# Kernel tuning notes

Measured on AMD Instinct MI355X. Metric: run time of the kernel, lower is better.

Reference implementation:

```python
import jax, jax.numpy as jnp
import numpy as np

V, B, T, D, H, HS, L, F = 50257, 16, 256, 64, 4, 16, 4, 256
EPS = 1e-5


def layernorm(x, g, b):
    mu = jnp.mean(x, axis=-1, keepdims=True)
    var = jnp.var(x, axis=-1, keepdims=True)
    return (x - mu) * jax.lax.rsqrt(var + EPS) * g + b


def setup_inputs() -> dict:
    key = jax.random.key(0)
    ks = jax.random.split(key, 20)
    s = 0.02
    inp = {
        "idx": jax.random.randint(ks[0], (B, T), 0, V),
        "targets": jax.random.randint(ks[1], (B, T), 0, V),
        "tok_emb": jax.random.normal(ks[2], (V, D), jnp.float32) * s,
        "pos_emb": jax.random.normal(ks[3], (T, D), jnp.float32) * s,
        "Wq": jax.random.normal(ks[4], (L, H, D, HS), jnp.float32) * s,
        "Wk": jax.random.normal(ks[5], (L, H, D, HS), jnp.float32) * s,
        "Wv": jax.random.normal(ks[6], (L, H, D, HS), jnp.float32) * s,
        "Wo": jax.random.normal(ks[7], (L, D, D), jnp.float32) * s,
        "bo": jnp.zeros((L, D), jnp.float32),
        "ln1_g": jnp.ones((L, D), jnp.float32),
        "ln1_b": jnp.zeros((L, D), jnp.float32),
        "ln2_g": jnp.ones((L, D), jnp.float32),
        "ln2_b": jnp.zeros((L, D), jnp.float32),
        "W1": jax.random.normal(ks[8], (L, D, F), jnp.float32) * s,
        "b1": jnp.zeros((L, F), jnp.float32),
        "W2": jax.random.normal(ks[9], (L, F, D), jnp.float32) * s,
        "b2": jnp.zeros((L, D), jnp.float32),
        "lnf_g": jnp.ones((D,), jnp.float32),
        "lnf_b": jnp.zeros((D,), jnp.float32),
        "Whead": jax.random.normal(ks[10], (D, V), jnp.float32) * s,
        "bhead": jnp.zeros((V,), jnp.float32),
    }
    return inp


def reference(idx, targets, tok_emb, pos_emb, Wq, Wk, Wv, Wo, bo,
              ln1_g, ln1_b, ln2_g, ln2_b, W1, b1, W2, b2,
              lnf_g, lnf_b, Whead, bhead):
    Tt = idx.shape[1]
    x = tok_emb[idx] + pos_emb[:Tt]  # [B,T,D]
    causal = jnp.tril(jnp.ones((Tt, Tt), bool))
    for l in range(L):
        h = layernorm(x, ln1_g[l], ln1_b[l])
        q = jnp.einsum('btd,hds->bhts', h, Wq[l])
        k = jnp.einsum('btd,hds->bhts', h, Wk[l])
        v = jnp.einsum('btd,hds->bhts', h, Wv[l])
        # NOTE: original applies NO 1/sqrt(head_size) scaling
        scores = jnp.einsum('bhts,bhus->bhtu', q, k)  # [B,H,T,T]
        scores = jnp.where(causal, scores, -jnp.inf)
        attn = jax.nn.softmax(scores, axis=-1)
        o = jnp.einsum('bhtu,bhus->bths', attn, v)  # [B,T,H,HS]
        o = o.reshape(o.shape[0], Tt, D)
        x = x + o @ Wo[l] + bo[l]
        h2 = layernorm(x, ln2_g[l], ln2_b[l])
        x = x + jax.nn.relu(h2 @ W1[l] + b1[l]) @ W2[l] + b2[l]
    x = layernorm(x, lnf_g, lnf_b)
    logits = x @ Whead + bhead  # [B,T,V]
    logp = jax.nn.log_softmax(logits, axis=-1)
    loss = -jnp.mean(jnp.take_along_axis(logp, targets[..., None], axis=-1))
    return (logits, loss)
```

## Files before the change

### kernel.cpp

```cpp
#include <hip/hip_runtime.h>
#include <hip/hip_bf16.h>
#include <math.h>

constexpr int NV  = 50257;
constexpr int NB  = 16;
constexpr int NT  = 256;
constexpr int ND  = 64;
constexpr int NH  = 4;
constexpr int NHS = 16;
constexpr int NL  = 4;
constexpr int NF  = 256;
constexpr int NN  = NB * NT;
constexpr float EPS = 1e-5f;

constexpr int NCB2 = 200;
constexpr int NVP  = NCB2 * 256;
constexpr int LOGITS = NN * NV;
constexpr int RB_N  = NN / 64;
constexpr int CB_PER_XCD = NCB2 / 8;

constexpr int X_OFF   = 0;
constexpr int Q_OFF   = X_OFF  + NN * ND;
constexpr int K_OFF   = Q_OFF  + NN * ND;
constexpr int V_OFF   = K_OFF  + NN * ND;
constexpr int O_OFF   = V_OFF  + NN * ND;
constexpr int A_OFF   = O_OFF  + NN * ND;
constexpr int XFB_OFF = A_OFF  + NN * NF;
constexpr int WM_OFF  = XFB_OFF + NN * ND / 2;
constexpr int WS2_OFF = WM_OFF + 200 * NN;
constexpr int WHB_OFF = WS2_OFF + 200 * NN;
constexpr int LP_OFF  = WHB_OFF + NVP * 32;

typedef __bf16 bf16x8 __attribute__((ext_vector_type(8)));
typedef float  f32x4  __attribute__((ext_vector_type(4)));

__global__ __launch_bounds__(256) void k_ln_qkv(
        float* __restrict__ x, const float* __restrict__ g, const float* __restrict__ bb,
        const float* __restrict__ Wq, const float* __restrict__ Wk, const float* __restrict__ Wv,
        __hip_bfloat16* __restrict__ q, __hip_bfloat16* __restrict__ k,
        __hip_bfloat16* __restrict__ v,
        const int* __restrict__ idx, const float* __restrict__ tok,
        const float* __restrict__ pos) {
    __shared__ float hs[16][65];
    int t = threadIdx.x;
    int r0 = blockIdx.x * 16;
    for (int i = t; i < 16 * 64; i += 256) {
        int n = r0 + (i >> 6);
        int tt = n & (NT - 1), d = i & 63;
        float e = tok[idx[n] * ND + d] + pos[tt * ND + d];
        hs[i >> 6][i & 63] = e;
        x[(size_t)r0 * 64 + i] = e;
    }
    __syncthreads();
    {
        int row = t >> 4, sub = t & 15;
        float s = 0.f, s2 = 0.f;
        #pragma unroll
        for (int j = 0; j < 4; j++) { float vv = hs[row][sub * 4 + j]; s += vv; s2 += vv * vv; }
        #pragma unroll
        for (int off = 1; off < 16; off <<= 1) { s += __shfl_xor(s, off); s2 += __shfl_xor(s2, off); }
        float mu = s * (1.f / 64.f);
        float var = s2 * (1.f / 64.f) - mu * mu;
        float rs = rsqrtf(var + EPS);
        #pragma unroll
        for (int j = 0; j < 4; j++) {
            int d = sub * 4 + j;
            hs[row][d] = (hs[row][d] - mu) * rs * g[d] + bb[d];
        }
    }
    __syncthreads();
    int c = t & 63, rg = t >> 6;
    int head = c >> 4, sidx = c & 15;
    float aq[4], ak[4], av[4];
    #pragma unroll
    for (int i = 0; i < 4; i++) { aq[i] = 0.f; ak[i] = 0.f; av[i] = 0.f; }
    for (int kk = 0; kk < 64; kk++) {
        float wq = Wq[(head * 64 + kk) * 16 + sidx];
        float wk = Wk[(head * 64 + kk) * 16 + sidx];
        float wv = Wv[(head * 64 + kk) * 16 + sidx];
        #pragma unroll
        for (int i = 0; i < 4; i++) {
            float h = hs[rg * 4 + i][kk];
            aq[i] += h * wq; ak[i] += h * wk; av[i] += h * wv;
        }
    }
    #pragma unroll
    for (int i = 0; i < 4; i++) {
        int n = r0 + rg * 4 + i;
        int b = n >> 8, tt = n & 255;
        int oidx = ((b * NH + head) * NT + tt) * NHS + sidx;
        q[oidx] = __float2bfloat16(aq[i]);
        k[oidx] = __float2bfloat16(ak[i]);
        v[oidx] = __float2bfloat16(av[i]);
    }
}

__global__ __launch_bounds__(256) void k_attn(
        const __hip_bfloat16* __restrict__ q, const __hip_bfloat16* __restrict__ k,
        const __hip_bfloat16* __restrict__ v, float* __restrict__ o) {
    __shared__ __bf16 ks[256][24];
    __shared__ __bf16 vt[16][264];
    __shared__ __bf16 ps[4][16][40];

    int blk = blockIdx.x;
    int bh = blk >> 2, tq = blk & 3;
    int t = threadIdx.x;
    int w = t >> 6, l = t & 63;
    int lr = l & 15, lg = l >> 4;
    int nrows = tq * 64 + 64;

    const __hip_bfloat16* kbp = k + (size_t)bh * NT * NHS;
    const __hip_bfloat16* vbp = v + (size_t)bh * NT * NHS;
    for (int r = t; r < nrows; r += 256) {
        const uint4* src = (const uint4*)(kbp + r * 16);
        uint4 k0 = src[0], k1 = src[1];
        *(uint4*)&ks[r][0] = k0;
        *(uint4*)&ks[r][8] = k1;
        const uint4* vsrc = (const uint4*)(vbp + r * 16);
        union { uint4 u[2]; __bf16 h[16]; } vu;
        vu.u[0] = vsrc[0]; vu.u[1] = vsrc[1];
        #pragma unroll
        for (int hh = 0; hh < 16; hh++)
            vt[hh][r] = vu.h[hh];
    }
    __syncthreads();

    bf16x8 zero8;
    #pragma unroll
    for (int e = 0; e < 8; e++) zero8[e] = (__bf16)0.0f;

    int qb = tq * 64 + w * 16;
    bf16x8 qf = zero8;
    if (lg < 2)
        qf = *reinterpret_cast<const bf16x8*>(q + ((size_t)bh * NT + qb + lr) * 16 + lg * 8);

    int ntiles = tq * 4 + w + 1;
    f32x4 oacc = {0.f, 0.f, 0.f, 0.f};
    float lsum[4] = {0.f, 0.f, 0.f, 0.f};

    for (int kt = 0; kt < ntiles; kt++) {
        int kb2 = kt * 16;
        bool diag = (kt == ntiles - 1);

        bf16x8 kf = zero8;
        if (lg < 2)
            kf = *reinterpret_cast<const bf16x8*>(&ks[kb2 + lr][lg * 8]);

        f32x4 s4 = {0.f, 0.f, 0.f, 0.f};
        s4 = __builtin_amdgcn_mfma_f32_16x16x32_bf16(qf, kf, s4, 0, 0, 0);

        #pragma unroll
        for (int reg = 0; reg < 4; reg++) {
            float pv = __expf(s4[reg]);
            if (diag && lr > lg * 4 + reg) pv = 0.f;
            lsum[reg] += pv;
            ps[w][lg * 4 + reg][lr] = (__bf16)pv;
        }

        bf16x8 pf = zero8, vf = zero8;
        if (lg < 2) {
            pf = *reinterpret_cast<const bf16x8*>(&ps[w][lr][lg * 8]);
            vf = *reinterpret_cast<const bf16x8*>(&vt[lr][kb2 + lg * 8]);
        }
        oacc = __builtin_amdgcn_mfma_f32_16x16x32_bf16(pf, vf, oacc, 0, 0, 0);
    }

    #pragma unroll
    for (int reg = 0; reg < 4; reg++) {
        float e = lsum[reg];
        #pragma unroll
        for (int off = 1; off < 16; off <<= 1) e += __shfl_xor(e, off);
        lsum[reg] = e;
    }

    int b = bh >> 2, h = bh & 3;
    #pragma unroll
    for (int reg = 0; reg < 4; reg++) {
        int qrow = qb + lg * 4 + reg;
        o[((size_t)b * NT + qrow) * ND + h * NHS + lr] = oacc[reg] / lsum[reg];
    }
}

__global__ __launch_bounds__(256) void k_post(
        const float* __restrict__ o, const float* __restrict__ Wo, const float* __restrict__ bo,
        const float* __restrict__ g2, const float* __restrict__ bg2,
        const float* __restrict__ W1, const float* __restrict__ b1,
        const float* __restrict__ W2, const float* __restrict__ b2m,
        float* __restrict__ x,
        const float* __restrict__ g1n, const float* __restrict__ b1n,
        const float* __restrict__ Wqn, const float* __restrict__ Wkn,
        const float* __restrict__ Wvn,
        __hip_bfloat16* __restrict__ q, __hip_bfloat16* __restrict__ k,
        __hip_bfloat16* __restrict__ v,
        const float* __restrict__ lg, const float* __restrict__ lb,
        __hip_bfloat16* __restrict__ xfb, int last) {
    __shared__ float os[16][65];
    __shared__ float xs[16][65];
    __shared__ float as[16][257];
    int t = threadIdx.x;
    int r0 = blockIdx.x * 16;
    for (int i = t; i < 16 * 64; i += 256)
        os[i >> 6][i & 63] = o[r0 * 64 + i];
    __syncthreads();
    int c = t & 63, rg = t >> 6;
    {
        float pr[4] = {0.f, 0.f, 0.f, 0.f};
        for (int kk = 0; kk < 64; kk++) {
            float w = Wo[kk * 64 + c];
            #pragma unroll
            for (int i = 0; i < 4; i++) pr[i] += os[rg * 4 + i][kk] * w;
        }
        float bias = bo[c];
        #pragma unroll
        for (int i = 0; i < 4; i++) {
            int row = rg * 4 + i;
            xs[row][c] = x[(r0 + row) * 64 + c] + pr[i] + bias;
        }
    }
    __syncthreads();
    {
        int row = t >> 4, sub = t & 15;
        float s = 0.f, s2 = 0.f;
        #pragma unroll
        for (int j = 0; j < 4; j++) { float vv = xs[row][sub * 4 + j]; s += vv; s2 += vv * vv; }
        #pragma unroll
        for (int off = 1; off < 16; off <<= 1) { s += __shfl_xor(s, off); s2 += __shfl_xor(s2, off); }
        float mu = s * (1.f / 64.f);
        float var = s2 * (1.f / 64.f) - mu * mu;
        float rs = rsqrtf(var + EPS);
        #pragma unroll
        for (int j = 0; j < 4; j++) {
            int d = sub * 4 + j;
            os[row][d] = (xs[row][d] - mu) * rs * g2[d] + bg2[d];
        }
    }
    __syncthreads();
    {
        float m1[16];
        #pragma unroll
        for (int i = 0; i < 16; i++) m1[i] = 0.f;
        for (int kk = 0; kk < 64; kk++) {
            float w = W1[kk * NF + t];
            #pragma unroll
            for (int i = 0; i < 16; i++) m1[i] += os[i][kk] * w;
        }
        float bb1 = b1[t];
        #pragma unroll
        for (int i = 0; i < 16; i++) as[i][t] = fmaxf(m1[i] + bb1, 0.f);
    }
    __syncthreads();
    {
        float m2[4] = {0.f, 0.f, 0.f, 0.f};
        for (int kk = 0; kk < 256; kk++) {
            float w = W2[kk * 64 + c];
            #pragma unroll
            for (int i = 0; i < 4; i++) m2[i] += as[rg * 4 + i][kk] * w;
        }
        float bias = b2m[c];
        #pragma unroll
        for (int i = 0; i < 4; i++) {
            int row = rg * 4 + i;
            xs[row][c] += m2[i] + bias;
        }
    }
    __syncthreads();

    if (last) {
        int row = t >> 4, sub = t & 15;
        float s = 0.f, s2 = 0.f;
        #pragma unroll
        for (int j = 0; j < 4; j++) { float vv = xs[row][sub * 4 + j]; s += vv; s2 += vv * vv; }
        #pragma unroll
        for (int off = 1; off < 16; off <<= 1) { s += __shfl_xor(s, off); s2 += __shfl_xor(s2, off); }
        float mu = s * (1.f / 64.f);
        float var = s2 * (1.f / 64.f) - mu * mu;
        float rs = rsqrtf(var + EPS);
        #pragma unroll
        for (int j = 0; j < 4; j++) {
            int d = sub * 4 + j;
            float val = (xs[row][d] - mu) * rs * lg[d] + lb[d];
            xfb[(r0 + row) * 64 + d] = __float2bfloat16(val);
        }
        return;
    }

    {
        #pragma unroll
        for (int i = 0; i < 4; i++) {
            int row = rg * 4 + i;
            x[(r0 + row) * 64 + c] = xs[row][c];
        }
    }
    {
        int row = t >> 4, sub = t & 15;
        float s = 0.f, s2 = 0.f;
        #pragma unroll
        for (int j = 0; j < 4; j++) { float vv = xs[row][sub * 4 + j]; s += vv; s2 += vv * vv; }
        #pragma unroll
        for (int off = 1; off < 16; off <<= 1) { s += __shfl_xor(s, off); s2 += __shfl_xor(s2, off); }
        float mu = s * (1.f / 64.f);
        float var = s2 * (1.f / 64.f) - mu * mu;
        float rs = rsqrtf(var + EPS);
        #pragma unroll
        for (int j = 0; j < 4; j++) {
            int d = sub * 4 + j;
            os[row][d] = (xs[row][d] - mu) * rs * g1n[d] + b1n[d];
        }
    }
    __syncthreads();
    {
        int head = c >> 4, sidx = c & 15;
        float aq[4], ak[4], av[4];
        #pragma unroll
        for (int i = 0; i < 4; i++) { aq[i] = 0.f; ak[i] = 0.f; av[i] = 0.f; }
        for (int kk = 0; kk < 64; kk++) {
            float wq = Wqn[(head * 64 + kk) * 16 + sidx];
            float wk = Wkn[(head * 64 + kk) * 16 + sidx];
            float wv = Wvn[(head * 64 + kk) * 16 + sidx];
            #pragma unroll
            for (int i = 0; i < 4; i++) {
                float h = os[rg * 4 + i][kk];
                aq[i] += h * wq; ak[i] += h * wk; av[i] += h * wv;
            }
        }
        #pragma unroll
        for (int i = 0; i < 4; i++) {
            int n = r0 + rg * 4 + i;
            int b = n >> 8, tt = n & 255;
            int oidx = ((b * NH + head) * NT + tt) * NHS + sidx;
            q[oidx] = __float2bfloat16(aq[i]);
            k[oidx] = __float2bfloat16(ak[i]);
            v[oidx] = __float2bfloat16(av[i]);
        }
    }
}

__global__ __launch_bounds__(256) void k_convW(
        const float* __restrict__ Wh, __hip_bfloat16* __restrict__ whb) {
    __shared__ float w[64][65];
    int t = threadIdx.x;
    int n0 = blockIdx.x * 64;
    for (int i = t; i < 64 * 64; i += 256) {
        int k = i >> 6, c = i & 63;
        int n = n0 + c;
        w[k][c] = (n < NV) ? Wh[k * NV + n] : 0.f;
    }
    __syncthreads();
    int c = t >> 2, kq = t & 3;
    int n = n0 + c;
    union { __hip_bfloat16 h[16]; uint4 u[2]; } pk;
    #pragma unroll
    for (int j = 0; j < 16; j++)
        pk.h[j] = __float2bfloat16(w[kq * 16 + j][c]);
    uint4* dst = (uint4*)(whb + (size_t)n * 64 + kq * 16);
    dst[0] = pk.u[0];
    dst[1] = pk.u[1];
}

__global__ __launch_bounds__(256) void k_head(
        const __hip_bfloat16* __restrict__ xfb, const __hip_bfloat16* __restrict__ whb,
        const float* __restrict__ bhead, float* __restrict__ out,
        float* __restrict__ wsum) {
    __shared__ float ssm[4][64];

    int i0 = blockIdx.x;
    int xcd = i0 & 7;
    int j  = i0 >> 3;
    int rb = j / CB_PER_XCD;
    int cb = xcd * CB_PER_XCD + (j - rb * CB_PER_XCD);

    int t = threadIdx.x;
    int w = t >> 6, l = t & 63;
    int lr = l & 15, lg = l >> 4;
    int r0 = rb * 64;
    int cw = cb * 256 + w * 64;
    int c4 = cw + lr * 4;

    bf16x8 a[4][2], b[4][2];
    {
        const __hip_bfloat16* ap = xfb + (size_t)(r0 + lr) * 64 + lg * 8;
        #pragma unroll
        for (int m = 0; m < 4; m++)
            #pragma unroll
            for (int ks = 0; ks < 2; ks++)
                a[m][ks] = *reinterpret_cast<const bf16x8*>(ap + m * 16 * 64 + ks * 32);
        const __hip_bfloat16* bp = whb + (size_t)c4 * 64 + lg * 8;
        #pragma unroll
        for (int n = 0; n < 4; n++)
            #pragma unroll
            for (int ks = 0; ks < 2; ks++)
                b[n][ks] = *reinterpret_cast<const bf16x8*>(bp + n * 64 + ks * 32);
    }

    f32x4 acc[4][4];
    #pragma unroll
    for (int m = 0; m < 4; m++)
        #pragma unroll
        for (int n = 0; n < 4; n++)
            #pragma unroll
            for (int j2 = 0; j2 < 4; j2++) acc[m][n][j2] = 0.f;

    #pragma unroll
    for (int ks = 0; ks < 2; ks++)
        #pragma unroll
        for (int m = 0; m < 4; m++)
            #pragma unroll
            for (int n = 0; n < 4; n++)
                acc[m][n] = __builtin_amdgcn_mfma_f32_16x16x32_bf16(a[m][ks], b[n][ks], acc[m][n], 0, 0, 0);

    bool all4 = (c4 + 3 < NV);
    float bias[4];
    bool  cok[4];
    if (all4) {
        float4 bv = *(const float4*)(bhead + c4);
        bias[0] = bv.x; bias[1] = bv.y; bias[2] = bv.z; bias[3] = bv.w;
        cok[0] = cok[1] = cok[2] = cok[3] = true;
    } else {
        #pragma unroll
        for (int n = 0; n < 4; n++) {
            int gc = c4 + n;
            cok[n] = (gc < NV);
            bias[n] = cok[n] ? bhead[gc] : 0.f;
        }
    }

    float es[16];
    #pragma unroll
    for (int m = 0; m < 4; m++) {
        #pragma unroll
        for (int i = 0; i < 4; i++) {
            int rl = 4 * lg + i;
            int grow = r0 + m * 16 + rl;
            float vals[4];
            float e = 0.f;
            #pragma unroll
            for (int n = 0; n < 4; n++) {
                float v = acc[m][n][i] + bias[n];
                vals[n] = v;
                if (cok[n]) e += __expf(v);
            }
            es[m * 4 + i] = e;
            float* dst = out + (size_t)grow * NV + c4;
            if (all4) {
                f32x4 vv = {vals[0], vals[1], vals[2], vals[3]};
                __builtin_nontemporal_store(vv, (f32x4*)dst);
            } else {
                #pragma unroll
                for (int n = 0; n < 4; n++)
                    if (cok[n]) __builtin_nontemporal_store(vals[n], dst + n);
            }
        }
    }

    #pragma unroll
    for (int m = 0; m < 4; m++) {
        #pragma unroll
        for (int i = 0; i < 4; i++) {
            float e = es[m * 4 + i];
            #pragma unroll
            for (int off = 1; off < 16; off <<= 1) e += __shfl_xor(e, off);
            if (lr == 0) ssm[w][m * 16 + 4 * lg + i] = e;
        }
    }

    __syncthreads();
    if (t < 64)
        wsum[cb * NN + r0 + t] = ssm[0][t] + ssm[1][t] + ssm[2][t] + ssm[3][t];
}

__global__ void k_loss1(const float* __restrict__ wsum,
                        const float* __restrict__ out, const int* __restrict__ targets,
                        float* __restrict__ lp) {
    int row = blockIdx.x * blockDim.x + threadIdx.x;
    if (row >= NN) return;
    float S = 0.f;
    for (int cb = 0; cb < NCB2; cb++)
        S += wsum[cb * NN + row];
    float lse = logf(S);
    int tg = targets[row];
    float lt = out[(size_t)row * NV + tg];
    lp[row] = lt - lse;
}

__global__ void k_loss2(const float* __restrict__ lp, float* __restrict__ out) {
    __shared__ float red[4];
    int t = threadIdx.x;
    float s = 0.f;
    for (int i = t; i < NN; i += 256) s += lp[i];
    for (int off = 1; off < 64; off <<= 1) s += __shfl_xor(s, off);
    if ((t & 63) == 0) red[t >> 6] = s;
    __syncthreads();
    if (t == 0) {
        float tot = red[0] + red[1] + red[2] + red[3];
        out[LOGITS] = -tot / (float)NN;
    }
}

extern "C" void kernel_launch(void* const* d_in, const int* in_sizes, int n_in,
                              void* d_out, int out_size, void* d_ws, size_t ws_size,
                              hipStream_t stream) {
    const int*   idx     = (const int*)d_in[0];
    const int*   targets = (const int*)d_in[1];
    const float* tok     = (const float*)d_in[2];
    const float* pos     = (const float*)d_in[3];
    const float* Wq      = (const float*)d_in[4];
    const float* Wk      = (const float*)d_in[5];
    const float* Wv      = (const float*)d_in[6];
    const float* Wo      = (const float*)d_in[7];
    const float* bo      = (const float*)d_in[8];
    const float* ln1g    = (const float*)d_in[9];
    const float* ln1b    = (const float*)d_in[10];
    const float* ln2g    = (const float*)d_in[11];
    const float* ln2b    = (const float*)d_in[12];
    const float* W1      = (const float*)d_in[13];
    const float* b1      = (const float*)d_in[14];
    const float* W2      = (const float*)d_in[15];
    const float* b2      = (const float*)d_in[16];
    const float* lnfg    = (const float*)d_in[17];
    const float* lnfb    = (const float*)d_in[18];
    const float* Wh      = (const float*)d_in[19];
    const float* bhead   = (const float*)d_in[20];

    float* ws = (float*)d_ws;
    float* x  = ws + X_OFF;
    __hip_bfloat16* q = (__hip_bfloat16*)(ws + Q_OFF);
    __hip_bfloat16* k = (__hip_bfloat16*)(ws + K_OFF);
    __hip_bfloat16* v = (__hip_bfloat16*)(ws + V_OFF);
    float* o  = ws + O_OFF;
    __hip_bfloat16* xfb = (__hip_bfloat16*)(ws + XFB_OFF);
    float* wsm = ws + WS2_OFF;
    __hip_bfloat16* whb = (__hip_bfloat16*)(ws + WHB_OFF);
    float* lp  = ws + LP_OFF;
    float* out = (float*)d_out;

    k_convW<<<NVP / 64, 256, 0, stream>>>(Wh, whb);

    k_ln_qkv<<<NN / 16, 256, 0, stream>>>(x, ln1g, ln1b, Wq, Wk, Wv, q, k, v,
                                          idx, tok, pos);

    for (int l = 0; l < NL; l++) {
        int last = (l == NL - 1) ? 1 : 0;
        int ln = last ? l : l + 1;
        k_attn<<<NB * NH * 4, 256, 0, stream>>>(q, k, v, o);
        k_post<<<NN / 16, 256, 0, stream>>>(o, Wo + l * ND * ND, bo + l * ND,
                                            ln2g + l * ND, ln2b + l * ND,
                                            W1 + l * ND * NF, b1 + l * NF,
                                            W2 + l * NF * ND, b2 + l * ND, x,
                                            ln1g + ln * ND, ln1b + ln * ND,
                                            Wq + ln * NH * ND * NHS,
                                            Wk + ln * NH * ND * NHS,
                                            Wv + ln * NH * ND * NHS,
                                            q, k, v,
                                            lnfg, lnfb, xfb, last);
    }

    k_head<<<NCB2 * RB_N, 256, 0, stream>>>(xfb, whb, bhead, out, wsm);

    k_loss1<<<NN / 256, 256, 0, stream>>>(wsm, out, targets, lp);
    k_loss2<<<1, 256, 0, stream>>>(lp, out);
}
```

Baseline: 495.5 us.

## Fuse attention into per-layer kernel with ping-pong QKV buffers and transposed V

Merges the separate attention kernel into the post-attention MLP kernel, so each 16-row block computes its own causal attention straight from global K/V. Q/K/V are double-buffered across layers to avoid races, and V is stored transposed so the PV MFMA operand loads are contiguous. This removes one launch per layer and the fp32 attention-output round trip through global memory. The cost is redundant K/V reads, since there is no LDS staging and each block rereads the K/V prefix. The head kernel also swaps nontemporal stores for plain stores and replaces the shuffle reduction with an LDS reduction.

After: 504.9 us. About the same (+1.9%).

```diff
diff --git a/kernel.cpp b/kernel.cpp
--- a/kernel.cpp
+++ b/kernel.cpp
@@ -25,6 +25,9 @@
 constexpr int V_OFF   = K_OFF  + NN * ND;
 constexpr int O_OFF   = V_OFF  + NN * ND;
 constexpr int A_OFF   = O_OFF  + NN * ND;
+constexpr int Q2_OFF  = O_OFF;
+constexpr int K2_OFF  = O_OFF + NN * ND / 2;
+constexpr int V2_OFF  = A_OFF;
 constexpr int XFB_OFF = A_OFF  + NN * NF;
 constexpr int WM_OFF  = XFB_OFF + NN * ND / 2;
 constexpr int WS2_OFF = WM_OFF + 200 * NN;
@@ -71,6 +74,7 @@
     __syncthreads();
     int c = t & 63, rg = t >> 6;
     int head = c >> 4, sidx = c & 15;
+    int b = r0 >> 8, tt0 = r0 & 255;
     float aq[4], ak[4], av[4];
     #pragma unroll
     for (int i = 0; i < 4; i++) { aq[i] = 0.f; ak[i] = 0.f; av[i] = 0.f; }
@@ -86,103 +90,23 @@
     }
     #pragma unroll
     for (int i = 0; i < 4; i++) {
-        int n = r0 + rg * 4 + i;
-        int b = n >> 8, tt = n & 255;
+        int tt = tt0 + rg * 4 + i;
         int oidx = ((b * NH + head) * NT + tt) * NHS + sidx;
         q[oidx] = __float2bfloat16(aq[i]);
         k[oidx] = __float2bfloat16(ak[i]);
-        v[oidx] = __float2bfloat16(av[i]);
-    }
-}
-
-__global__ __launch_bounds__(256) void k_attn(
-        const __hip_bfloat16* __restrict__ q, const __hip_bfloat16* __restrict__ k,
-        const __hip_bfloat16* __restrict__ v, float* __restrict__ o) {
-    __shared__ __bf16 ks[256][24];
-    __shared__ __bf16 vt[16][264];
-    __shared__ __bf16 ps[4][16][40];
-
-    int blk = blockIdx.x;
-    int bh = blk >> 2, tq = blk & 3;
-    int t = threadIdx.x;
-    int w = t >> 6, l = t & 63;
-    int lr = l & 15, lg = l >> 4;
-    int nrows = tq * 64 + 64;
-
-    const __hip_bfloat16* kbp = k + (size_t)bh * NT * NHS;
-    const __hip_bfloat16* vbp = v + (size_t)bh * NT * NHS;
-    for (int r = t; r < nrows; r += 256) {
-        const uint4* src = (const uint4*)(kbp + r * 16);
-        uint4 k0 = src[0], k1 = src[1];
-        *(uint4*)&ks[r][0] = k0;
-        *(uint4*)&ks[r][8] = k1;
-        const uint4* vsrc = (const uint4*)(vbp + r * 16);
-        union { uint4 u[2]; __bf16 h[16]; } vu;
-        vu.u[0] = vsrc[0]; vu.u[1] = vsrc[1];
-        #pragma unroll
-        for (int hh = 0; hh < 16; hh++)
-            vt[hh][r] = vu.h[hh];
-    }
-    __syncthreads();
-
-    bf16x8 zero8;
-    #pragma unroll
-    for (int e = 0; e < 8; e++) zero8[e] = (__bf16)0.0f;
-
-    int qb = tq * 64 + w * 16;
-    bf16x8 qf = zero8;
-    if (lg < 2)
-        qf = *reinterpret_cast<const bf16x8*>(q + ((size_t)bh * NT + qb + lr) * 16 + lg * 8);
-
-    int ntiles = tq * 4 + w + 1;
-    f32x4 oacc = {0.f, 0.f, 0.f, 0.f};
-    float lsum[4] = {0.f, 0.f, 0.f, 0.f};
-
-    for (int kt = 0; kt < ntiles; kt++) {
-        int kb2 = kt * 16;
-        bool diag = (kt == ntiles - 1);
-
-        bf16x8 kf = zero8;
-        if (lg < 2)
-            kf = *reinterpret_cast<const bf16x8*>(&ks[kb2 + lr][lg * 8]);
-
-        f32x4 s4 = {0.f, 0.f, 0.f, 0.f};
-        s4 = __builtin_amdgcn_mfma_f32_16x16x32_bf16(qf, kf, s4, 0, 0, 0);
-
-        #pragma unroll
-        for (int reg = 0; reg < 4; reg++) {
-            float pv = __expf(s4[reg]);
-            if (diag && lr > lg * 4 + reg) pv = 0.f;
-            lsum[reg] += pv;
-            ps[w][lg * 4 + reg][lr] = (__bf16)pv;
-        }
-
-        bf16x8 pf = zero8, vf = zero8;
-        if (lg < 2) {
-            pf = *reinterpret_cast<const bf16x8*>(&ps[w][lr][lg * 8]);
-            vf = *reinterpret_cast<const bf16x8*>(&vt[lr][kb2 + lg * 8]);
-        }
-        oacc = __builtin_amdgcn_mfma_f32_16x16x32_bf16(pf, vf, oacc, 0, 0, 0);
-    }
-
-    #pragma unroll
-    for (int reg = 0; reg < 4; reg++) {
-        float e = lsum[reg];
-        #pragma unroll
-        for (int off = 1; off < 16; off <<= 1) e += __shfl_xor(e, off);
-        lsum[reg] = e;
-    }
-
-    int b = bh >> 2, h = bh & 3;
-    #pragma unroll
-    for (int reg = 0; reg < 4; reg++) {
-        int qrow = qb + lg * 4 + reg;
-        o[((size_t)b * NT + qrow) * ND + h * NHS + lr] = oacc[reg] / lsum[reg];
-    }
-}
-
-__global__ __launch_bounds__(256) void k_post(
-        const float* __restrict__ o, const float* __restrict__ Wo, const float* __restrict__ bo,
+    }
+    union { __hip_bfloat16 h[4]; unsigned long long u; } pv;
+    #pragma unroll
+    for (int i = 0; i < 4; i++) pv.h[i] = __float2bfloat16(av[i]);
+    *(unsigned long long*)(v + ((size_t)(b * NH + head) * NHS + sidx) * NT + tt0 + rg * 4) = pv.u;
+}
+
+__global__ __launch_bounds__(256) void k_layer(
+        const __hip_bfloat16* __restrict__ qi, const __hip_bfloat16* __restrict__ ki,
+        const __hip_bfloat16* __restrict__ vi,
+        __hip_bfloat16* __restrict__ qo, __hip_bfloat16* __restrict__ ko,
+        __hip_bfloat16* __restrict__ vo,
+        const float* __restrict__ Wo, const float* __restrict__ bo,
         const float* __restrict__ g2, const float* __restrict__ bg2,
         const float* __restrict__ W1, const float* __restrict__ b1,
         const float* __restrict__ W2, const float* __restrict__ b2m,
@@ -190,25 +114,77 @@
         const float* __restrict__ g1n, const float* __restrict__ b1n,
         const float* __restrict__ Wqn, const float* __restrict__ Wkn,
         const float* __restrict__ Wvn,
-        __hip_bfloat16* __restrict__ q, __hip_bfloat16* __restrict__ k,
-        __hip_bfloat16* __restrict__ v,
-        const float* __restrict__ lg, const float* __restrict__ lb,
+        const float* __restrict__ lgf, const float* __restrict__ lbf,
         __hip_bfloat16* __restrict__ xfb, int last) {
+    __shared__ __bf16 ps[4][16][40];
     __shared__ float os[16][65];
     __shared__ float xs[16][65];
     __shared__ float as[16][257];
+
     int t = threadIdx.x;
+    int w = t >> 6, l = t & 63;
+    int lr = l & 15, lgp = l >> 4;
     int r0 = blockIdx.x * 16;
-    for (int i = t; i < 16 * 64; i += 256)
-        os[i >> 6][i & 63] = o[r0 * 64 + i];
-    __syncthreads();
+    int b = r0 >> 8, tt0 = r0 & 255;
+
+    bf16x8 zero8;
+    #pragma unroll
+    for (int e = 0; e < 8; e++) zero8[e] = (__bf16)0.0f;
+
+    bf16x8 qf = zero8;
+    if (lgp < 2)
+        qf = *reinterpret_cast<const bf16x8*>(qi + ((size_t)(b * NH + w) * NT + tt0 + lr) * NHS + lgp * 8);
+
+    int ntiles = (tt0 >> 4) + 1;
+    f32x4 oacc = {0.f, 0.f, 0.f, 0.f};
+    float lsum[4] = {0.f, 0.f, 0.f, 0.f};
+
+    for (int kt = 0; kt < ntiles; kt++) {
+        int kb = kt * 16;
+        bool diag = (kt == ntiles - 1);
+
+        bf16x8 kf = zero8;
+        if (lgp < 2)
+            kf = *reinterpret_cast<const bf16x8*>(ki + ((size_t)(b * NH + w) * NT + kb + lr) * NHS + lgp * 8);
+
+        f32x4 s4 = {0.f, 0.f, 0.f, 0.f};
+        s4 = __builtin_amdgcn_mfma_f32_16x16x32_bf16(qf, kf, s4, 0, 0, 0);
+
+        #pragma unroll
+        for (int reg = 0; reg < 4; reg++) {
+            float pv = __expf(s4[reg]);
+            if (diag && lr > lgp * 4 + reg) pv = 0.f;
+            lsum[reg] += pv;
+            ps[w][lgp * 4 + reg][lr] = (__bf16)pv;
+        }
+
+        bf16x8 pf = zero8, vf = zero8;
+        if (lgp < 2) {
+            pf = *reinterpret_cast<const bf16x8*>(&ps[w][lr][lgp * 8]);
+            vf = *reinterpret_cast<const bf16x8*>(vi + ((size_t)(b * NH + w) * NHS + lr) * NT + kb + lgp * 8);
+        }
+        oacc = __builtin_amdgcn_mfma_f32_16x16x32_bf16(pf, vf, oacc, 0, 0, 0);
+    }
+
+    #pragma unroll
+    for (int reg = 0; reg < 4; reg++) {
+        float e = lsum[reg];
+        #pragma unroll
+        for (int off = 1; off < 16; off <<= 1) e += __shfl_xor(e, off);
+        lsum[reg] = e;
+    }
+    #pragma unroll
+    for (int reg = 0; reg < 4; reg++)
+        os[lgp * 4 + reg][w * 16 + lr] = oacc[reg] / lsum[reg];
+    __syncthreads();
+
     int c = t & 63, rg = t >> 6;
     {
         float pr[4] = {0.f, 0.f, 0.f, 0.f};
         for (int kk = 0; kk < 64; kk++) {
-            float w = Wo[kk * 64 + c];
-            #pragma unroll
-            for (int i = 0; i < 4; i++) pr[i] += os[rg * 4 + i][kk] * w;
+            float ww = Wo[kk * 64 + c];
+            #pragma unroll
+            for (int i = 0; i < 4; i++) pr[i] += os[rg * 4 + i][kk] * ww;
         }
         float bias = bo[c];
         #pragma unroll
@@ -240,9 +216,9 @@
         #pragma unroll
         for (int i = 0; i < 16; i++) m1[i] = 0.f;
         for (int kk = 0; kk < 64; kk++) {
-            float w = W1[kk * NF + t];
-            #pragma unroll
-            for (int i = 0; i < 16; i++) m1[i] += os[i][kk] * w;
+            float ww = W1[kk * NF + t];
+            #pragma unroll
+            for (int i = 0; i < 16; i++) m1[i] += os[i][kk] * ww;
         }
         float bb1 = b1[t];
         #pragma unroll
@@ -252,9 +228,9 @@
     {
         float m2[4] = {0.f, 0.f, 0.f, 0.f};
         for (int kk = 0; kk < 256; kk++) {
-            float w = W2[kk * 64 + c];
-            #pragma unroll
-            for (int i = 0; i < 4; i++) m2[i] += as[rg * 4 + i][kk] * w;
+            float ww = W2[kk * 64 + c];
+            #pragma unroll
+            for (int i = 0; i < 4; i++) m2[i] += as[rg * 4 + i][kk] * ww;
         }
         float bias = b2m[c];
         #pragma unroll
@@ -278,7 +254,7 @@
         #pragma unroll
         for (int j = 0; j < 4; j++) {
             int d = sub * 4 + j;
-            float val = (xs[row][d] - mu) * rs * lg[d] + lb[d];
+            float val = (xs[row][d] - mu) * rs * lgf[d] + lbf[d];
             xfb[(r0 + row) * 64 + d] = __float2bfloat16(val);
         }
         return;
@@ -325,13 +301,15 @@
         }
         #pragma unroll
         for (int i = 0; i < 4; i++) {
-            int n = r0 + rg * 4 + i;
-            int b = n >> 8, tt = n & 255;
+            int tt = tt0 + rg * 4 + i;
             int oidx = ((b * NH + head) * NT + tt) * NHS + sidx;
-            q[oidx] = __float2bfloat16(aq[i]);
-            k[oidx] = __float2bfloat16(ak[i]);
-            v[oidx] = __float2bfloat16(av[i]);
-        }
+            qo[oidx] = __float2bfloat16(aq[i]);
+            ko[oidx] = __float2bfloat16(ak[i]);
+        }
+        union { __hip_bfloat16 h[4]; unsigned long long u; } pv;
+        #pragma unroll
+        for (int i = 0; i < 4; i++) pv.h[i] = __float2bfloat16(av[i]);
+        *(unsigned long long*)(vo + ((size_t)(b * NH + head) * NHS + sidx) * NT + tt0 + rg * 4) = pv.u;
     }
 }
 
@@ -361,7 +339,8 @@
         const __hip_bfloat16* __restrict__ xfb, const __hip_bfloat16* __restrict__ whb,
         const float* __restrict__ bhead, float* __restrict__ out,
         float* __restrict__ wsum) {
-    __shared__ float ssm[4][64];
+    __shared__ float pes[4][64][17];
+    __shared__ float ssm2[4][64];
 
     int i0 = blockIdx.x;
     int xcd = i0 & 7;
@@ -424,7 +403,6 @@
         }
     }
 
-    float es[16];
     #pragma unroll
     for (int m = 0; m < 4; m++) {
         #pragma unroll
@@ -439,33 +417,30 @@
                 vals[n] = v;
                 if (cok[n]) e += __expf(v);
             }
-            es[m * 4 + i] = e;
+            pes[w][m * 16 + rl][lr] = e;
             float* dst = out + (size_t)grow * NV + c4;
             if (all4) {
                 f32x4 vv = {vals[0], vals[1], vals[2], vals[3]};
-                __builtin_nontemporal_store(vv, (f32x4*)dst);
+                *(f32x4*)dst = vv;
             } else {
                 #pragma unroll
                 for (int n = 0; n < 4; n++)
-                    if (cok[n]) __builtin_nontemporal_store(vals[n], dst + n);
+                    if (cok[n]) dst[n] = vals[n];
             }
         }
     }
 
-    #pragma unroll
-    for (int m = 0; m < 4; m++) {
-        #pragma unroll
-        for (int i = 0; i < 4; i++) {
-            float e = es[m * 4 + i];
-            #pragma unroll
-            for (int off = 1; off < 16; off <<= 1) e += __shfl_xor(e, off);
-            if (lr == 0) ssm[w][m * 16 + 4 * lg + i] = e;
-        }
-    }
-
+    __syncthreads();
+    {
+        int w2 = t >> 6, row = t & 63;
+        float s = 0.f;
+        #pragma unroll
+        for (int k2 = 0; k2 < 16; k2++) s += pes[w2][row][k2];
+        ssm2[w2][row] = s;
+    }
     __syncthreads();
     if (t < 64)
-        wsum[cb * NN + r0 + t] = ssm[0][t] + ssm[1][t] + ssm[2][t] + ssm[3][t];
+        wsum[cb * NN + r0 + t] = ssm2[0][t] + ssm2[1][t] + ssm2[2][t] + ssm2[3][t];
 }
 
 __global__ void k_loss1(const float* __restrict__ wsum,
@@ -523,10 +498,12 @@
 
     float* ws = (float*)d_ws;
     float* x  = ws + X_OFF;
-    __hip_bfloat16* q = (__hip_bfloat16*)(ws + Q_OFF);
-    __hip_bfloat16* k = (__hip_bfloat16*)(ws + K_OFF);
-    __hip_bfloat16* v = (__hip_bfloat16*)(ws + V_OFF);
-    float* o  = ws + O_OFF;
+    __hip_bfloat16* q1 = (__hip_bfloat16*)(ws + Q_OFF);
+    __hip_bfloat16* k1 = (__hip_bfloat16*)(ws + K_OFF);
+    __hip_bfloat16* v1 = (__hip_bfloat16*)(ws + V_OFF);
+    __hip_bfloat16* q2 = (__hip_bfloat16*)(ws + Q2_OFF);
+    __hip_bfloat16* k2 = (__hip_bfloat16*)(ws + K2_OFF);
+    __hip_bfloat16* v2 = (__hip_bfloat16*)(ws + V2_OFF);
     __hip_bfloat16* xfb = (__hip_bfloat16*)(ws + XFB_OFF);
     float* wsm = ws + WS2_OFF;
     __hip_bfloat16* whb = (__hip_bfloat16*)(ws + WHB_OFF);
@@ -535,23 +512,25 @@
 
     k_convW<<<NVP / 64, 256, 0, stream>>>(Wh, whb);
 
-    k_ln_qkv<<<NN / 16, 256, 0, stream>>>(x, ln1g, ln1b, Wq, Wk, Wv, q, k, v,
+    k_ln_qkv<<<NN / 16, 256, 0, stream>>>(x, ln1g, ln1b, Wq, Wk, Wv, q1, k1, v1,
                                           idx, tok, pos);
 
     for (int l = 0; l < NL; l++) {
         int last = (l == NL - 1) ? 1 : 0;
         int ln = last ? l : l + 1;
-        k_attn<<<NB * NH * 4, 256, 0, stream>>>(q, k, v, o);
-        k_post<<<NN / 16, 256, 0, stream>>>(o, Wo + l * ND * ND, bo + l * ND,
-                                            ln2g + l * ND, ln2b + l * ND,
-                                            W1 + l * ND * NF, b1 + l * NF,
-                                            W2 + l * NF * ND, b2 + l * ND, x,
-                                            ln1g + ln * ND, ln1b + ln * ND,
-                                            Wq + ln * NH * ND * NHS,
-                                            Wk + ln * NH * ND * NHS,
-                                            Wv + ln * NH * ND * NHS,
-                                            q, k, v,
-                                            lnfg, lnfb, xfb, last);
+        __hip_bfloat16 *qi, *ki, *vi, *qo, *ko, *vo;
+        if (l & 1) { qi = q2; ki = k2; vi = v2; qo = q1; ko = k1; vo = v1; }
+        else       { qi = q1; ki = k1; vi = v1; qo = q2; ko = k2; vo = v2; }
+        k_layer<<<NN / 16, 256, 0, stream>>>(qi, ki, vi, qo, ko, vo,
+                                             Wo + l * ND * ND, bo + l * ND,
+                                             ln2g + l * ND, ln2b + l * ND,
+                                             W1 + l * ND * NF, b1 + l * NF,
+                                             W2 + l * NF * ND, b2 + l * ND, x,
+                                             ln1g + ln * ND, ln1b + ln * ND,
+                                             Wq + ln * NH * ND * NHS,
+                                             Wk + ln * NH * ND * NHS,
+                                             Wv + ln * NH * ND * NHS,
+                                             lnfg, lnfb, xfb, last);
     }
 
     k_head<<<NCB2 * RB_N, 256, 0, stream>>>(xfb, whb, bhead, out, wsm);
```
